# Performance work log

Hardware: AMD Instinct MI355X
Metric: run time of the kernel (lower is better)

## Reference

```python
import jax, jax.numpy as jnp
import numpy as np

QMAX = 127.0   # 8-bit symmetric quantization
BN_EPS = 1e-5
MID = 576      # in_channels * 6 expansion


def act_fake_quant(x):
    """Per-tensor symmetric 8-bit fake-quant of activations (HAWQ QuantAct).
    Returns dequantized value and the scaling factor. STE for gradients."""
    s = jax.lax.stop_gradient(jnp.max(jnp.abs(x)) / QMAX + 1e-8)
    q = jnp.clip(jnp.round(x / s), -QMAX, QMAX) * s
    return x + jax.lax.stop_gradient(q - x), s


def fold_bn(w, gamma, beta, mean, var):
    """Fold BN into conv weights/bias (QuantBnConv2d.set_param math)."""
    f = gamma / jnp.sqrt(var + BN_EPS)
    return w * f[:, None, None, None], beta - mean * f


def weight_fake_quant(w):
    """Per-output-channel symmetric 8-bit fake-quant of folded weights."""
    s = jax.lax.stop_gradient(jnp.max(jnp.abs(w), axis=(1, 2, 3)) / QMAX + 1e-8)
    sb = s[:, None, None, None]
    q = jnp.clip(jnp.round(w / sb), -QMAX, QMAX) * sb
    return w + jax.lax.stop_gradient(q - w), s


def qbn_conv(x, w, gamma, beta, mean, var, stride, groups, pad):
    """BN-folded, weight-quantized conv (QuantBnConv2d forward)."""
    wf, bf = fold_bn(w, gamma, beta, mean, var)
    wq, ws = weight_fake_quant(wf)
    y = jax.lax.conv_general_dilated(
        x, wq, window_strides=(stride, stride), padding=pad,
        dimension_numbers=('NCHW', 'OIHW', 'NCHW'), feature_group_count=groups)
    return y + bf[None, :, None, None], ws


def setup_inputs() -> dict:
    key = jax.random.key(0)
    ks = jax.random.split(key, 16)
    C_in, C_out = 96, 96
    d = {'x': jax.random.normal(ks[0], (64, C_in, 28, 28), jnp.float32)}
    def bn(k, c):
        k1, k2, k3, k4 = jax.random.split(k, 4)
        return (1.0 + 0.1 * jax.random.normal(k1, (c,), jnp.float32),   # gamma
                0.1 * jax.random.normal(k2, (c,), jnp.float32),          # beta
                0.1 * jax.random.normal(k3, (c,), jnp.float32),          # running mean
                0.5 + jax.random.uniform(k4, (c,), jnp.float32))         # running var
    # conv1: 1x1 expansion 96 -> 576
    d['w1'] = 0.1 * jax.random.normal(ks[1], (MID, C_in, 1, 1), jnp.float32)
    d['g1'], d['b1'], d['m1'], d['v1'] = bn(ks[2], MID)
    # conv2: 3x3 depthwise, groups=576
    d['w2'] = 0.1 * jax.random.normal(ks[3], (MID, 1, 3, 3), jnp.float32)
    d['g2'], d['b2'], d['m2'], d['v2'] = bn(ks[4], MID)
    # conv3: 1x1 projection 576 -> 96
    d['w3'] = 0.1 * jax.random.normal(ks[5], (C_out, MID, 1, 1), jnp.float32)
    d['g3'], d['b3'], d['m3'], d['v3'] = bn(ks[6], C_out)
    return d


def reference(x, w1, g1, b1, m1, v1, w2, g2, b2, m2, v2, w3, g3, b3, m3, v3):
    identity = x
    # quant_act on input
    y, act_sf = act_fake_quant(x)
    # conv1 (1x1 expansion) + ReLU6 + quant_act1
    y, _ = qbn_conv(y, w1, g1, b1, m1, v1, stride=1, groups=1, pad='VALID')
    y = jnp.clip(y, 0.0, 6.0)
    y, _ = act_fake_quant(y)
    # conv2 (3x3 depthwise) + ReLU6 + quant_act2
    y, _ = qbn_conv(y, w2, g2, b2, m2, v2, stride=1, groups=MID,
                    pad=((1, 1), (1, 1)))
    y = jnp.clip(y, 0.0, 6.0)
    y, _ = act_fake_quant(y)
    # conv3 (1x1 projection, linear)
    y, _ = qbn_conv(y, w3, g3, b3, m3, v3, stride=1, groups=1, pad='VALID')
    # residual add + quant_act_int32 requantization
    y = y + identity
    y, out_sf = act_fake_quant(y)
    return y, out_sf
```

## Files before the change

kernel.cpp:

```cpp
#include <hip/hip_runtime.h>
#include <hip/hip_fp16.h>

#define CIN   96
#define MIDC  576
#define COUT  96
#define HW    784
#define W28   28
#define NX    4816896

typedef __attribute__((ext_vector_type(8))) short short8;
typedef __attribute__((ext_vector_type(4))) float floatx4;


__device__ __forceinline__ float wave_max64(float v){
  #pragma unroll
  for(int i=32;i>=1;i>>=1) v = fmaxf(v, __shfl_xor(v, i, 64));
  return v;
}

__device__ __forceinline__ void block_max_atomic(float v, unsigned* dst){
  v = wave_max64(v);
  __shared__ float sm[8];
  int lane = threadIdx.x & 63, w = threadIdx.x >> 6;
  if(lane==0) sm[w] = v;
  __syncthreads();
  if(threadIdx.x==0){
    int nw = (blockDim.x + 63) >> 6;
    float m = sm[0];
    for(int i=1;i<nw;i++) m = fmaxf(m, sm[i]);
    atomicMax(dst, __float_as_uint(m));
  }
}

__device__ __forceinline__ float fq(float x, float s){
  float q = rintf(x / s);
  q = fminf(fmaxf(q, -127.f), 127.f);
  return q * s;
}

__device__ __forceinline__ float qint(float x, float s){
  return fminf(fmaxf(rintf(x / s), -127.f), 127.f);
}

__device__ __forceinline__ float qintr(float x, float r){
  return fminf(fmaxf(rintf(x * r), -127.f), 127.f);
}

__device__ __forceinline__ ushort f2bf(float f){
  return (ushort)(__float_as_uint(f) >> 16);
}


__global__ __launch_bounds__(256) void k_prep(
    const float* __restrict__ w1,const float* __restrict__ g1,const float* __restrict__ b1,const float* __restrict__ m1,const float* __restrict__ v1,
    const float* __restrict__ w2,const float* __restrict__ g2,const float* __restrict__ b2,const float* __restrict__ m2,const float* __restrict__ v2,
    const float* __restrict__ w3,const float* __restrict__ g3,const float* __restrict__ b3,const float* __restrict__ m3,const float* __restrict__ v3,
    ushort* __restrict__ qw1, float* __restrict__ sc1, float* __restrict__ bq1,
    float*  __restrict__ wq2, float* __restrict__ bq2,
    ushort* __restrict__ qw3, float* __restrict__ sc3, float* __restrict__ bq3,
    const float4* __restrict__ xv, unsigned* umax)
{
  int b = blockIdx.x, tid = threadIdx.x;
  if(b >= 1248){
    float m = 0.f;
    for(int i = (b-1248)*256 + tid; i < NX/4; i += 512*256){
      float4 v = xv[i];
      m = fmaxf(m, fmaxf(fmaxf(fabsf(v.x), fabsf(v.y)), fmaxf(fabsf(v.z), fabsf(v.w))));
    }
    block_max_atomic(m, umax);
    return;
  }
  if(tid >= 64) return;
  int lane = tid;
  if(b < MIDC){
    int o = b;
    float f = g1[o] / sqrtf(v1[o] + 1e-5f);
    float x0 = w1[o*CIN + lane] * f;
    float x1 = (lane < 32) ? w1[o*CIN + 64 + lane] * f : 0.f;
    float m = wave_max64(fmaxf(fabsf(x0), fabsf(x1)));
    float s = m / 127.f + 1e-8f;
    qw1[o*CIN + lane] = f2bf(qint(x0, s));
    if(lane < 32) qw1[o*CIN + 64 + lane] = f2bf(qint(x1, s));
    if(lane==0){ sc1[o] = s; bq1[o] = b1[o] - m1[o]*f; }
  } else if(b < 2*MIDC){
    int c = b - MIDC;
    float f = g2[c] / sqrtf(v2[c] + 1e-5f);
    float x0 = (lane < 9) ? w2[c*9 + lane] * f : 0.f;
    float m = wave_max64(fabsf(x0));
    float s = m / 127.f + 1e-8f;
    if(lane < 9) wq2[c*9 + lane] = fq(x0, s);
    if(lane==0) bq2[c] = b2[c] - m2[c]*f;
  } else {
    int o = b - 2*MIDC;
    float f = g3[o] / sqrtf(v3[o] + 1e-5f);
    float xs[9]; float m = 0.f;
    #pragma unroll
    for(int k=0;k<9;k++){ int c = lane + 64*k; xs[k] = w3[o*MIDC + c] * f; m = fmaxf(m, fabsf(xs[k])); }
    m = wave_max64(m);
    float s = m / 127.f + 1e-8f;
    #pragma unroll
    for(int k=0;k<9;k++){ int c = lane + 64*k; qw3[o*MIDC + c] = f2bf(qint(xs[k], s)); }
    if(lane==0){ sc3[o] = s; bq3[o] = b3[o] - m3[o]*f; }
  }
}

__global__ __launch_bounds__(384) void k_conv1f(const float* __restrict__ x,
    const ushort* __restrict__ qw1, const float* __restrict__ sc1, const float* __restrict__ bq1,
    unsigned* umax, __half* __restrict__ y1T)
{
  __shared__ ushort bt[12*64*8];
  int n = blockIdx.x, pc = blockIdx.y, tid = threadIdx.x;
  int w = tid >> 6, l = tid & 63;
  int lhi = l >> 4, llo = l & 15;
  int p0 = pc*56;
  float s0 = __uint_as_float(umax[0])/127.f + 1e-8f;
  float r0 = 1.f/s0;
  if(tid < 96){
    int cb = tid >> 3, px = 56 + (tid & 7);
    uint4 z; z.x=0u; z.y=0u; z.z=0u; z.w=0u;
    *(uint4*)(bt + (cb*64 + px)*8) = z;
  }
  for(int i = tid; i < 96*14; i += 384){
    int c = i/14, q = i - c*14;
    float4 v = *(const float4*)(x + (size_t)(n*CIN + c)*HW + p0 + q*4);
    int cb = c >> 3, c8 = c & 7;
    ushort* bp = bt + (cb*64 + q*4)*8 + c8;
    bp[0]  = f2bf(qintr(v.x, r0));
    bp[8]  = f2bf(qintr(v.y, r0));
    bp[16] = f2bf(qintr(v.z, r0));
    bp[24] = f2bf(qintr(v.w, r0));
  }
  __syncthreads();
  float tmax = 0.f;
  for(int mt=0; mt<6; mt++){
    int m0 = mt*96 + w*16;
    short8 a[3];
    #pragma unroll
    for(int ks=0; ks<3; ks++)
      a[ks] = *(const short8*)(qw1 + (m0 + llo)*CIN + ks*32 + lhi*8);
    float scf[4], bf[4];
    #pragma unroll
    for(int r=0;r<4;r++){ int o = m0 + lhi*4 + r; scf[r] = s0*sc1[o]; bf[r] = bq1[o]; }
    floatx4 acc[4];
    #pragma unroll
    for(int f=0;f<4;f++) acc[f] = (floatx4){0.f,0.f,0.f,0.f};
    #pragma unroll
    for(int ks=0; ks<3; ks++){
      #pragma unroll
      for(int f=0; f<4; f++){
        const short8 b = *(const short8*)(bt + ((ks*4 + lhi)*64 + f*16 + llo)*8);
        acc[f] = __builtin_amdgcn_mfma_f32_16x16x32_bf16(a[ks], b, acc[f], 0, 0, 0);
      }
    }
    int cgbase = (m0 >> 3) + (lhi >> 1);
    int c8base = (lhi & 1) * 4;
    #pragma unroll
    for(int f=0; f<4; f++){
      if(f*16 + llo < 56){
        uint pk0 = 0, pk1 = 0;
        #pragma unroll
        for(int r=0;r<4;r++){
          float v = fmaf(acc[f][r], scf[r], bf[r]);
          v = fminf(fmaxf(v, 0.f), 6.f);
          tmax = fmaxf(tmax, v);
          uint hb = (uint)__half_as_ushort(__float2half(v));
          if(r==0) pk0 = hb;        else if(r==1) pk0 |= hb<<16;
          else if(r==2) pk1 = hb;   else pk1 |= hb<<16;
        }
        uint2 pk; pk.x = pk0; pk.y = pk1;
        *(uint2*)((ushort*)y1T + ((size_t)(n*72 + cgbase)*HW + p0 + f*16 + llo)*8 + c8base) = pk;
      }
    }
  }
  block_max_atomic(tmax, umax + 1);
}

__global__ __launch_bounds__(256) void k_conv2(const __half* __restrict__ y1T,
    const float* __restrict__ wq2, const float* __restrict__ bq2,
    unsigned* umax, __half* __restrict__ y2T)
{
  __shared__ ushort tile[2][30*30*8];
  int cg = blockIdx.x >> 4, nb = (blockIdx.x & 15) << 2;
  int tid = threadIdx.x;
  float s1 = __uint_as_float(umax[1])/127.f + 1e-8f;
  float r1 = 1.f/s1;
  const float* wc = wq2 + cg*72;
  const float* bc = bq2 + cg*8;
  float tmax = 0.f;

  #pragma unroll
  for(int bfi=0; bfi<2; bfi++){
    uint4* t4z = (uint4*)tile[bfi];
    if(tid < 116){
      int h, w;
      if(tid < 30){ h = 0; w = tid; }
      else if(tid < 60){ h = 29; w = tid - 30; }
      else if(tid < 88){ h = tid - 59; w = 0; }
      else { h = tid - 87; w = 29; }
      t4z[h*30 + w] = (uint4){0u,0u,0u,0u};
    }
  }

  uint4 ld[4];
  {
    const uint4* g4 = (const uint4*)(y1T + (size_t)(nb*72 + cg)*HW*8);
    #pragma unroll
    for(int i=0;i<4;i++){ int p = tid + i*256; if(p < HW) ld[i] = g4[p]; }
    uint4* t4 = (uint4*)tile[0];
    #pragma unroll
    for(int i=0;i<4;i++){
      int p = tid + i*256;
      if(p < HW){
        int h = p/W28, w = p - h*W28;
        uint rw[4] = {ld[i].x, ld[i].y, ld[i].z, ld[i].w};
        uint pk[4];
        #pragma unroll
        for(int j=0;j<4;j++){
          float lo = __half2float(__ushort_as_half((ushort)(rw[j] & 0xffffu)));
          float hi = __half2float(__ushort_as_half((ushort)(rw[j] >> 16)));
          uint qlo = (uint)__half_as_ushort(__float2half(rintf(lo * r1)));
          uint qhi = (uint)__half_as_ushort(__float2half(rintf(hi * r1)));
          pk[j] = (qhi << 16) | qlo;
        }
        t4[(h+1)*30 + (w+1)] = (uint4){pk[0], pk[1], pk[2], pk[3]};
      }
    }
  }

  int cur = 0;
  for(int it=0; it<4; it++){
    int n = nb + it;
    if(it < 3){
      const uint4* g4 = (const uint4*)(y1T + (size_t)((n+1)*72 + cg)*HW*8);
      #pragma unroll
      for(int i=0;i<4;i++){ int p = tid + i*256; if(p < HW) ld[i] = g4[p]; }
    }
    __syncthreads();
    const uint4* t4 = (const uint4*)tile[cur];
    uint4* o4 = (uint4*)(y2T + (size_t)(n*72 + cg)*HW*8);
    #pragma unroll
    for(int i=0;i<4;i++){
      int p = tid + i*256;
      if(p < HW){
        int h = p/W28, w = p - h*W28;
        float acc[8];
        #pragma unroll
        for(int c=0;c<8;c++) acc[c] = 0.f;
        #pragma unroll
        for(int dy=0; dy<3; dy++){
          #pragma unroll
          for(int dx=0; dx<3; dx++){
            uint4 v = t4[(h+dy)*30 + (w+dx)];
            uint rw[4] = {v.x, v.y, v.z, v.w};
            #pragma unroll
            for(int j=0;j<4;j++){
              float lo = __half2float(__ushort_as_half((ushort)(rw[j] & 0xffffu)));
              float hi = __half2float(__ushort_as_half((ushort)(rw[j] >> 16)));
              acc[2*j]   = fmaf(lo, wc[(2*j)*9   + dy*3 + dx], acc[2*j]);
              acc[2*j+1] = fmaf(hi, wc[(2*j+1)*9 + dy*3 + dx], acc[2*j+1]);
            }
          }
        }
        uint pk[4];
        #pragma unroll
        for(int j=0;j<4;j++){
          float o0 = fmaf(acc[2*j],   s1, bc[2*j]);
          float o1 = fmaf(acc[2*j+1], s1, bc[2*j+1]);
          o0 = fminf(fmaxf(o0, 0.f), 6.f);
          o1 = fminf(fmaxf(o1, 0.f), 6.f);
          tmax = fmaxf(tmax, fmaxf(o0, o1));
          uint lo = (uint)__half_as_ushort(__float2half(o0));
          uint hi = (uint)__half_as_ushort(__float2half(o1));
          pk[j] = (hi << 16) | lo;
        }
        o4[p] = (uint4){pk[0], pk[1], pk[2], pk[3]};
      }
    }
    if(it < 3){
      uint4* t4n = (uint4*)tile[cur ^ 1];
      #pragma unroll
      for(int i=0;i<4;i++){
        int p = tid + i*256;
        if(p < HW){
          int h = p/W28, w = p - h*W28;
          uint rw[4] = {ld[i].x, ld[i].y, ld[i].z, ld[i].w};
          uint pk[4];
          #pragma unroll
          for(int j=0;j<4;j++){
            float lo = __half2float(__ushort_as_half((ushort)(rw[j] & 0xffffu)));
            float hi = __half2float(__ushort_as_half((ushort)(rw[j] >> 16)));
            uint qlo = (uint)__half_as_ushort(__float2half(rintf(lo * r1)));
            uint qhi = (uint)__half_as_ushort(__float2half(rintf(hi * r1)));
            pk[j] = (qhi << 16) | qlo;
          }
          t4n[(h+1)*30 + (w+1)] = (uint4){pk[0], pk[1], pk[2], pk[3]};
        }
      }
    }
    cur ^= 1;
  }
  block_max_atomic(tmax, umax + 2);
}

__global__ __launch_bounds__(384) void k_conv3(const __half* __restrict__ y2T,
    const ushort* __restrict__ qw3, const float* __restrict__ sc3, const float* __restrict__ bq3,
    const float* __restrict__ x, unsigned* umax, float* __restrict__ out)
{
  __shared__ ushort lds[24*64*8];
  int n = blockIdx.x, pc = blockIdx.y, tid = threadIdx.x;
  int w = tid >> 6, l = tid & 63;
  int lhi = l >> 4, llo = l & 15;
  int m0 = w*16;
  int p0 = pc*56;
  float s2 = __uint_as_float(umax[2])/127.f + 1e-8f;
  float r2 = 1.f/s2;
  uint4* l4 = (uint4*)lds;
  if(tid < 192){
    int cl = tid >> 3, px = 56 + (tid & 7);
    l4[cl*64 + px] = (uint4){0u,0u,0u,0u};
  }
  float scf[4], bf[4];
  #pragma unroll
  for(int r=0;r<4;r++){ int o = m0 + lhi*4 + r; scf[r] = s2*sc3[o]; bf[r] = bq3[o]; }
  floatx4 acc[4];
  #pragma unroll
  for(int f=0;f<4;f++) acc[f] = (floatx4){0.f,0.f,0.f,0.f};

  uint4 ld[4];
  #pragma unroll
  for(int i=0;i<4;i++){
    int idx = tid + i*384;
    if(idx < 24*56){
      int cl = idx/56, r = idx - cl*56;
      ld[i] = *(const uint4*)((const ushort*)y2T + ((size_t)(n*72 + cl)*HW + p0 + r)*8);
    }
  }
  for(int ck=0; ck<3; ck++){
    if(ck > 0) __syncthreads();
    #pragma unroll
    for(int i=0;i<4;i++){
      int idx = tid + i*384;
      if(idx < 24*56){
        int cl = idx/56, r = idx - cl*56;
        uint rw[4] = {ld[i].x, ld[i].y, ld[i].z, ld[i].w};
        uint pk[4];
        #pragma unroll
        for(int j=0;j<4;j++){
          float lo = __half2float(__ushort_as_half((ushort)(rw[j] & 0xffffu)));
          float hi = __half2float(__ushort_as_half((ushort)(rw[j] >> 16)));
          uint qlo = (uint)f2bf(rintf(lo * r2));
          uint qhi = (uint)f2bf(rintf(hi * r2));
          pk[j] = (qhi << 16) | qlo;
        }
        l4[cl*64 + r] = (uint4){pk[0], pk[1], pk[2], pk[3]};
      }
    }
    if(ck < 2){
      #pragma unroll
      for(int i=0;i<4;i++){
        int idx = tid + i*384;
        if(idx < 24*56){
          int cl = idx/56, r = idx - cl*56;
          ld[i] = *(const uint4*)((const ushort*)y2T + ((size_t)(n*72 + (ck+1)*24 + cl)*HW + p0 + r)*8);
        }
      }
    }
    __syncthreads();
    #pragma unroll
    for(int ks=0; ks<6; ks++){
      const short8 a = *(const short8*)(qw3 + (m0 + llo)*MIDC + ck*192 + ks*32 + lhi*8);
      #pragma unroll
      for(int f=0; f<4; f++){
        const short8 b = *(const short8*)(lds + ((ks*4 + lhi)*64 + f*16 + llo)*8);
        acc[f] = __builtin_amdgcn_mfma_f32_16x16x32_bf16(a, b, acc[f], 0, 0, 0);
      }
    }
  }
  float tmax = 0.f;
  #pragma unroll
  for(int f=0; f<4; f++){
    if(f*16 + llo < 56){
      #pragma unroll
      for(int r=0;r<4;r++){
        size_t idx = (size_t)(n*COUT + m0 + lhi*4 + r)*HW + p0 + f*16 + llo;
        float v = fmaf(acc[f][r], scf[r], bf[r]) + x[idx];
        tmax = fmaxf(tmax, fabsf(v));
        out[idx] = v;
      }
    }
  }
  block_max_atomic(tmax, umax + 3);
}

__global__ void k_finalq(float* __restrict__ out, const unsigned* __restrict__ umax, float* __restrict__ sf){
  int i = blockIdx.x*256 + threadIdx.x;
  float s3 = __uint_as_float(umax[3]) / 127.f + 1e-8f;
  float4* o4 = (float4*)out;
  float4 v = o4[i];
  v.x = fq(v.x, s3); v.y = fq(v.y, s3); v.z = fq(v.z, s3); v.w = fq(v.w, s3);
  o4[i] = v;
  if(i == 0) *sf = s3;
}


extern "C" void kernel_launch(void* const* d_in, const int* in_sizes, int n_in,
                              void* d_out, int out_size, void* d_ws, size_t ws_size,
                              hipStream_t stream)
{
  const float* x  = (const float*)d_in[0];
  const float* w1 = (const float*)d_in[1];
  const float* g1 = (const float*)d_in[2];
  const float* b1 = (const float*)d_in[3];
  const float* m1 = (const float*)d_in[4];
  const float* v1 = (const float*)d_in[5];
  const float* w2 = (const float*)d_in[6];
  const float* g2 = (const float*)d_in[7];
  const float* b2 = (const float*)d_in[8];
  const float* m2 = (const float*)d_in[9];
  const float* v2 = (const float*)d_in[10];
  const float* w3 = (const float*)d_in[11];
  const float* g3 = (const float*)d_in[12];
  const float* b3 = (const float*)d_in[13];
  const float* m3 = (const float*)d_in[14];
  const float* v3 = (const float*)d_in[15];

  char* ws = (char*)d_ws;
  unsigned* umax = (unsigned*)(ws + 0);
  float* sc1  = (float*)(ws + 256);
  float* bq1  = (float*)(ws + 2560);
  float* bq2  = (float*)(ws + 4864);
  float* wq2  = (float*)(ws + 7168);
  float* sc3  = (float*)(ws + 27904);
  float* bq3  = (float*)(ws + 28288);
  ushort* qw1 = (ushort*)(ws + 28672);
  ushort* qw3 = (ushort*)(ws + 139264);
  __half* y1T = (__half*)(ws + 9883648);
  __half* y2T = (__half*)(ws + 67686400);

  float* outp = (float*)d_out;

  hipMemsetAsync(umax, 0, 16, stream);
  k_prep<<<1760, 256, 0, stream>>>(w1,g1,b1,m1,v1, w2,g2,b2,m2,v2, w3,g3,b3,m3,v3,
                                   qw1,sc1,bq1, wq2,bq2, qw3,sc3,bq3,
                                   (const float4*)x, umax);
  k_conv1f<<<dim3(64,14), 384, 0, stream>>>(x, qw1, sc1, bq1, umax, y1T);
  k_conv2<<<1152, 256, 0, stream>>>(y1T, wq2, bq2, umax, y2T);
  k_conv3<<<dim3(64,14), 384, 0, stream>>>(y2T, qw3, sc3, bq3, x, umax, outp);
  k_finalq<<<NX/4/256, 256, 0, stream>>>(outp, umax, outp + NX);
}
```

Measured before the change: 117.9 us.

## Register-block depthwise conv over 4 pixels and pack prep blocks four waves each

```diff
diff --git a/kernel.cpp b/kernel.cpp
--- a/kernel.cpp
+++ b/kernel.cpp
@@ -61,19 +61,18 @@
     const float4* __restrict__ xv, unsigned* umax)
 {
   int b = blockIdx.x, tid = threadIdx.x;
-  if(b >= 1248){
+  if(b >= 312){
     float m = 0.f;
-    for(int i = (b-1248)*256 + tid; i < NX/4; i += 512*256){
+    for(int i = (b-312)*256 + tid; i < NX/4; i += 512*256){
       float4 v = xv[i];
       m = fmaxf(m, fmaxf(fmaxf(fabsf(v.x), fabsf(v.y)), fmaxf(fabsf(v.z), fabsf(v.w))));
     }
     block_max_atomic(m, umax);
     return;
   }
-  if(tid >= 64) return;
-  int lane = tid;
-  if(b < MIDC){
-    int o = b;
+  int w = tid >> 6, lane = tid & 63;
+  if(b < 144){
+    int o = b*4 + w;
     float f = g1[o] / sqrtf(v1[o] + 1e-5f);
     float x0 = w1[o*CIN + lane] * f;
     float x1 = (lane < 32) ? w1[o*CIN + 64 + lane] * f : 0.f;
@@ -82,8 +81,8 @@
     qw1[o*CIN + lane] = f2bf(qint(x0, s));
     if(lane < 32) qw1[o*CIN + 64 + lane] = f2bf(qint(x1, s));
     if(lane==0){ sc1[o] = s; bq1[o] = b1[o] - m1[o]*f; }
-  } else if(b < 2*MIDC){
-    int c = b - MIDC;
+  } else if(b < 288){
+    int c = (b-144)*4 + w;
     float f = g2[c] / sqrtf(v2[c] + 1e-5f);
     float x0 = (lane < 9) ? w2[c*9 + lane] * f : 0.f;
     float m = wave_max64(fabsf(x0));
@@ -91,7 +90,7 @@
     if(lane < 9) wq2[c*9 + lane] = fq(x0, s);
     if(lane==0) bq2[c] = b2[c] - m2[c]*f;
   } else {
-    int o = b - 2*MIDC;
+    int o = (b-288)*4 + w;
     float f = g3[o] / sqrtf(v3[o] + 1e-5f);
     float xs[9]; float m = 0.f;
     #pragma unroll
@@ -115,11 +114,6 @@
   int p0 = pc*56;
   float s0 = __uint_as_float(umax[0])/127.f + 1e-8f;
   float r0 = 1.f/s0;
-  if(tid < 96){
-    int cb = tid >> 3, px = 56 + (tid & 7);
-    uint4 z; z.x=0u; z.y=0u; z.z=0u; z.w=0u;
-    *(uint4*)(bt + (cb*64 + px)*8) = z;
-  }
   for(int i = tid; i < 96*14; i += 384){
     int c = i/14, q = i - c*14;
     float4 v = *(const float4*)(x + (size_t)(n*CIN + c)*HW + p0 + q*4);
@@ -238,34 +232,48 @@
     __syncthreads();
     const uint4* t4 = (const uint4*)tile[cur];
     uint4* o4 = (uint4*)(y2T + (size_t)(n*72 + cg)*HW*8);
-    #pragma unroll
-    for(int i=0;i<4;i++){
-      int p = tid + i*256;
-      if(p < HW){
-        int h = p/W28, w = p - h*W28;
-        float acc[8];
-        #pragma unroll
-        for(int c=0;c<8;c++) acc[c] = 0.f;
-        #pragma unroll
-        for(int dy=0; dy<3; dy++){
+    if(tid < 196){
+      int pq = tid*4;
+      int h = pq/W28, w0 = pq - h*W28;
+      float acc[4][8];
+      #pragma unroll
+      for(int k=0;k<4;k++)
+        #pragma unroll
+        for(int c=0;c<8;c++) acc[k][c] = 0.f;
+      #pragma unroll
+      for(int dy=0; dy<3; dy++){
+        uint4 t[6];
+        #pragma unroll
+        for(int j=0;j<6;j++) t[j] = t4[(h+dy)*30 + (w0+j)];
+        #pragma unroll
+        for(int j=0;j<6;j++){
+          float f8[8];
+          uint rw[4] = {t[j].x, t[j].y, t[j].z, t[j].w};
           #pragma unroll
-          for(int dx=0; dx<3; dx++){
-            uint4 v = t4[(h+dy)*30 + (w+dx)];
-            uint rw[4] = {v.x, v.y, v.z, v.w};
-            #pragma unroll
-            for(int j=0;j<4;j++){
-              float lo = __half2float(__ushort_as_half((ushort)(rw[j] & 0xffffu)));
-              float hi = __half2float(__ushort_as_half((ushort)(rw[j] >> 16)));
-              acc[2*j]   = fmaf(lo, wc[(2*j)*9   + dy*3 + dx], acc[2*j]);
-              acc[2*j+1] = fmaf(hi, wc[(2*j+1)*9 + dy*3 + dx], acc[2*j+1]);
+          for(int u=0;u<4;u++){
+            f8[2*u]   = __half2float(__ushort_as_half((ushort)(rw[u] & 0xffffu)));
+            f8[2*u+1] = __half2float(__ushort_as_half((ushort)(rw[u] >> 16)));
+          }
+          int klo = (j >= 3) ? (j-2) : 0;
+          int khi = (j < 4) ? j : 3;
+          #pragma unroll
+          for(int k=0;k<4;k++){
+            if(k >= klo && k <= khi){
+              int dx = j - k;
+              #pragma unroll
+              for(int c=0;c<8;c++)
+                acc[k][c] = fmaf(f8[c], wc[c*9 + dy*3 + dx], acc[k][c]);
             }
           }
         }
+      }
+      #pragma unroll
+      for(int k=0;k<4;k++){
         uint pk[4];
         #pragma unroll
         for(int j=0;j<4;j++){
-          float o0 = fmaf(acc[2*j],   s1, bc[2*j]);
-          float o1 = fmaf(acc[2*j+1], s1, bc[2*j+1]);
+          float o0 = fmaf(acc[k][2*j],   s1, bc[2*j]);
+          float o1 = fmaf(acc[k][2*j+1], s1, bc[2*j+1]);
           o0 = fminf(fmaxf(o0, 0.f), 6.f);
           o1 = fminf(fmaxf(o1, 0.f), 6.f);
           tmax = fmaxf(tmax, fmaxf(o0, o1));
@@ -273,7 +281,7 @@
           uint hi = (uint)__half_as_ushort(__float2half(o1));
           pk[j] = (hi << 16) | lo;
         }
-        o4[p] = (uint4){pk[0], pk[1], pk[2], pk[3]};
+        o4[pq + k] = (uint4){pk[0], pk[1], pk[2], pk[3]};
       }
     }
     if(it < 3){
@@ -315,10 +323,6 @@
   float s2 = __uint_as_float(umax[2])/127.f + 1e-8f;
   float r2 = 1.f/s2;
   uint4* l4 = (uint4*)lds;
-  if(tid < 192){
-    int cl = tid >> 3, px = 56 + (tid & 7);
-    l4[cl*64 + px] = (uint4){0u,0u,0u,0u};
-  }
   float scf[4], bf[4];
   #pragma unroll
   for(int r=0;r<4;r++){ int o = m0 + lhi*4 + r; scf[r] = s2*sc3[o]; bf[r] = bq3[o]; }
@@ -440,9 +444,9 @@
   float* outp = (float*)d_out;
 
   hipMemsetAsync(umax, 0, 16, stream);
-  k_prep<<<1760, 256, 0, stream>>>(w1,g1,b1,m1,v1, w2,g2,b2,m2,v2, w3,g3,b3,m3,v3,
-                                   qw1,sc1,bq1, wq2,bq2, qw3,sc3,bq3,
-                                   (const float4*)x, umax);
+  k_prep<<<824, 256, 0, stream>>>(w1,g1,b1,m1,v1, w2,g2,b2,m2,v2, w3,g3,b3,m3,v3,
+                                  qw1,sc1,bq1, wq2,bq2, qw3,sc3,bq3,
+                                  (const float4*)x, umax);
   k_conv1f<<<dim3(64,14), 384, 0, stream>>>(x, qw1, sc1, bq1, umax, y1T);
   k_conv2<<<1152, 256, 0, stream>>>(y1T, wq2, bq2, umax, y2T);
   k_conv3<<<dim3(64,14), 384, 0, stream>>>(y2T, qw3, sc3, bq3, x, umax, outp);
```

Measured after the change: 118.7 us. No clear change (+0.6%).
